# Kernel tuning notes

Hardware: AMD Instinct MI355X
Metric: run time of the kernel (lower is better)

The kernel has to match this reference:

```python
import jax, jax.numpy as jnp
import numpy as np

B, NMAX, H, C, HID = 256, 512, 256, 64, 512
NEG = jnp.float32(-1e9)

def setup_inputs() -> dict:
    key = jax.random.key(0)
    ks = jax.random.split(key, 12)
    s_in = 1.0 / np.sqrt(2 * H + C)
    s_h = 1.0 / np.sqrt(HID)
    return {
        "nodes_hv": jax.random.normal(ks[0], (B, NMAX, H), jnp.float32),
        "class_cond": jax.random.normal(ks[1], (B, C), jnp.float32),
        "W1": jax.random.normal(ks[2], (2 * H + C, HID), jnp.float32) * s_in,
        "b1": jnp.zeros((HID,), jnp.float32),
        "W2": jax.random.normal(ks[3], (HID, HID), jnp.float32) * s_h,
        "b2": jnp.zeros((HID,), jnp.float32),
        "W3": jax.random.normal(ks[4], (HID, 1), jnp.float32) * s_h,
        "b3": jnp.zeros((1,), jnp.float32),
        "dirns": jax.random.randint(ks[5], (B,), 0, 2, jnp.int32),
        "node_counts": jax.random.randint(ks[6], (B,), NMAX // 2 + 1, NMAX, jnp.int32),
        "dests": jax.random.randint(ks[7], (B,), 0, NMAX // 2, jnp.int32),
    }

def reference(nodes_hv, class_cond, W1, b1, W2, b2, W3, b3, dirns, node_counts, dests):
    Bb, Nmax, Hh = nodes_hv.shape
    D = Nmax - 1  # padded number of candidate destinations
    # per-graph newest node embedding: hv[b, n_b - 1]
    src_idx = (node_counts - 1).astype(jnp.int32)
    src_embed = jnp.take_along_axis(nodes_hv, src_idx[:, None, None], axis=1)  # [B,1,H]
    src_b = jnp.broadcast_to(src_embed, (Bb, D, Hh))
    cand = nodes_hv[:, :D, :]  # candidate (old-node) embeddings, padded
    # dirn == 1: edge new->old, so (src_side, dest_side) = (cand, new); else (new, cand)
    dirn1 = (dirns == 1)[:, None, None]
    side_a = jnp.where(dirn1, cand, src_b)
    side_b = jnp.where(dirn1, src_b, cand)
    cc = jnp.broadcast_to(class_cond[:, None, :], (Bb, D, class_cond.shape[-1]))
    x = jnp.concatenate([side_a, side_b, cc], axis=2)  # [B, D, 2H+C]
    h = jax.nn.relu(jnp.einsum("bdi,ih->bdh", x, W1) + b1)
    h = jax.nn.relu(jnp.einsum("bdi,ih->bdh", h, W2) + b2)
    scores = (jnp.einsum("bdi,io->bdo", h, W3) + b3)[..., 0]  # [B, D]
    # ragged validity: graph b has n_b - 1 candidates
    valid = jnp.arange(D)[None, :] < (node_counts - 1)[:, None]
    scores = jnp.where(valid, scores, NEG)
    logp = jax.nn.log_softmax(scores, axis=1)
    loss = -jnp.take_along_axis(logp, dests[:, None].astype(jnp.int32), axis=1)[:, 0]  # [B]
    return loss
```

## Files before the change

### kernel.cpp

```cpp
#include <hip/hip_runtime.h>
#include <math.h>

#define BB    256
#define NMAX  512
#define HH    256
#define CC    64
#define HID   512
#define NEGV  -1000000000.0f
#define MT    64
#define NW    8
#define SA_LD 258
#define TILE  512
#define KSTR  (16 * TILE)

typedef __attribute__((ext_vector_type(8)))  short  short8;
typedef __attribute__((ext_vector_type(16))) float  floatx16;

__device__ inline ushort f2bf(float x) {
    unsigned u = __float_as_uint(x);
    u = (u + 0x7FFFu + ((u >> 16) & 1u)) >> 16;
    return (ushort)u;
}

__global__ __launch_bounds__(256) void prep_kernel(
    const float* __restrict__ W1, const float* __restrict__ W2,
    ushort* __restrict__ Wt1s, ushort* __restrict__ Wt2s,
    const float* __restrict__ nodes_hv, const float* __restrict__ class_cond,
    const float* __restrict__ b1,
    const int* __restrict__ dirns, const int* __restrict__ node_counts,
    float* __restrict__ v_ws)
{
    const int blk = blockIdx.x;
    const int t = threadIdx.x;

    __shared__ float s_conv[32][68];
    __shared__ float s_src[HH];
    __shared__ float s_cc[CC];

    if (blk < 256) {
        const float* W = (blk < 128) ? W1 : W2;
        ushort* out    = (blk < 128) ? Wt1s : Wt2s;
        const int bb  = blk & 127;
        const int kb  = bb >> 3, ntg = bb & 7;

        {
            const int kl = t >> 3, nn = (t & 7) * 8;
            const float* src = W + (size_t)(kb * 32 + kl) * HID + ntg * 64 + nn;
            *(float4*)&s_conv[kl][nn]     = *(const float4*)src;
            *(float4*)&s_conv[kl][nn + 4] = *(const float4*)(src + 4);
        }
        __syncthreads();

        const int tile_l = t >> 6, ls = t & 63;
        const int kh_l = tile_l >> 1, nt_l = tile_l & 1;
        const int q5s = ls >> 5, l31s = ls & 31;
        short8 o;
        #pragma unroll
        for (int j = 0; j < 8; ++j)
            o[j] = (short)f2bf(s_conv[kh_l * 16 + q5s * 8 + j][nt_l * 32 + l31s]);
        const int kh = kb * 2 + kh_l, nt = ntg * 2 + nt_l;
        *(short8*)(out + ((size_t)kh * 16 + nt) * TILE + ls * 8) = o;
    } else {
        const int b = blk - 256;
        const int nc   = node_counts[b];
        const int dirn = dirns[b];
        const int src_idx = nc - 1;

        s_src[t] = nodes_hv[((size_t)b * NMAX + src_idx) * HH + t];
        if (t < CC) s_cc[t] = class_cond[b * CC + t];
        __syncthreads();

        const int srcoff = (dirn == 1) ? HH : 0;

        const int j = 2 * t;
        float acc0 = b1[j];
        float acc1 = b1[j + 1];

        #pragma unroll 4
        for (int r = 0; r < HH; ++r) {
            const float s = s_src[r];
            const float* wp = W1 + (size_t)(srcoff + r) * HID + j;
            acc0 += s * wp[0];
            acc1 += s * wp[1];
        }
        #pragma unroll 4
        for (int c = 0; c < CC; ++c) {
            const float s = s_cc[c];
            const float* wp = W1 + (size_t)(2 * HH + c) * HID + j;
            acc0 += s * wp[0];
            acc1 += s * wp[1];
        }
        v_ws[b * HID + j]     = acc0;
        v_ws[b * HID + j + 1] = acc1;
    }
}

__global__ __launch_bounds__(512, 4) void mlp2(
    const float* __restrict__ nodes_hv,
    const ushort* __restrict__ Wt1s, const ushort* __restrict__ Wt2s,
    const float* __restrict__ b2, const float* __restrict__ W3,
    const float* __restrict__ b3,
    const int* __restrict__ dirns, const int* __restrict__ node_counts,
    const float* __restrict__ v_ws, float* __restrict__ scores)
{
    const int b  = blockIdx.y;
    const int d0 = blockIdx.x * MT;
    const int t  = threadIdx.x;
    const int lane = t & 63, wv = t >> 6;
    const int l31 = lane & 31, q5 = lane >> 5;

    __shared__ ushort s_u[32768];

    const int nc = node_counts[b];

    if (d0 >= nc - 1) {
        if (t < MT) scores[b * NMAX + d0 + t] = NEGV;
        return;
    }

    const int kh0 = (dirns[b] == 1) ? 0 : 16;

    {
        const float4* src4 = (const float4*)nodes_hv + ((size_t)b * NMAX + d0) * (HH / 4);
        #pragma unroll
        for (int i = 0; i < (MT * HH / 4) / 512; ++i) {
            int idx = t + i * 512;
            int row = idx >> 6, c4 = idx & 63;
            float4 v = src4[idx];
            ushort4 p;
            p.x = f2bf(v.x); p.y = f2bf(v.y); p.z = f2bf(v.z); p.w = f2bf(v.w);
            *(ushort4*)&s_u[row * SA_LD + c4 * 4] = p;
        }
    }
    __syncthreads();

    floatx16 acc[2][2];
    #pragma unroll
    for (int mt = 0; mt < 2; ++mt)
        #pragma unroll
        for (int nt = 0; nt < 2; ++nt)
            #pragma unroll
            for (int r = 0; r < 16; ++r)
                acc[mt][nt][r] = 0.f;

    {
        const ushort* wb1 = Wt1s + ((size_t)kh0 * 16 + wv * 2) * TILE + lane * 8;
        #pragma unroll
        for (int kh = 0; kh < 16; ++kh) {
            const ushort* wp = wb1 + (size_t)kh * KSTR;
            short8 b0 = *(const short8*)(wp);
            short8 b1f = *(const short8*)(wp + TILE);
            short8 a0 = *(const short8*)&s_u[(l31)      * SA_LD + kh * 16 + q5 * 8];
            short8 a1 = *(const short8*)&s_u[(32 + l31) * SA_LD + kh * 16 + q5 * 8];
            acc[0][0] = __builtin_amdgcn_mfma_f32_32x32x16_bf16(a0, b0,  acc[0][0], 0, 0, 0);
            acc[0][1] = __builtin_amdgcn_mfma_f32_32x32x16_bf16(a0, b1f, acc[0][1], 0, 0, 0);
            acc[1][0] = __builtin_amdgcn_mfma_f32_32x32x16_bf16(a1, b0,  acc[1][0], 0, 0, 0);
            acc[1][1] = __builtin_amdgcn_mfma_f32_32x32x16_bf16(a1, b1f, acc[1][1], 0, 0, 0);
        }
    }
    __syncthreads();

    {
        #pragma unroll
        for (int nt = 0; nt < 2; ++nt) {
            const int n = wv * 64 + nt * 32 + l31;
            const float v = v_ws[b * HID + n];
            const int kh2 = n >> 4;
            const int q2p = (n >> 3) & 1;
            const int j_w = n & 7;
            #pragma unroll
            for (int mt = 0; mt < 2; ++mt) {
                #pragma unroll
                for (int reg = 0; reg < 16; ++reg) {
                    const int l31w = (reg & 3) + 8 * (reg >> 2) + 4 * q5;
                    float h = acc[mt][nt][reg] + v;
                    h = h > 0.f ? h : 0.f;
                    s_u[((kh2 * 2 + mt) * 64 + q2p * 32 + l31w) * 8 + j_w] = f2bf(h);
                }
            }
        }
    }
    __syncthreads();

    #pragma unroll
    for (int mt = 0; mt < 2; ++mt)
        #pragma unroll
        for (int nt = 0; nt < 2; ++nt)
            #pragma unroll
            for (int r = 0; r < 16; ++r)
                acc[mt][nt][r] = 0.f;
    {
        const ushort* wb2 = Wt2s + ((size_t)wv * 2) * TILE + lane * 8;
        #pragma unroll
        for (int kh2 = 0; kh2 < 32; ++kh2) {
            const ushort* wp = wb2 + (size_t)kh2 * KSTR;
            short8 b0 = *(const short8*)(wp);
            short8 b1f = *(const short8*)(wp + TILE);
            short8 a0 = *(const short8*)&s_u[((kh2 * 2 + 0) * 64 + lane) * 8];
            short8 a1 = *(const short8*)&s_u[((kh2 * 2 + 1) * 64 + lane) * 8];
            acc[0][0] = __builtin_amdgcn_mfma_f32_32x32x16_bf16(a0, b0,  acc[0][0], 0, 0, 0);
            acc[0][1] = __builtin_amdgcn_mfma_f32_32x32x16_bf16(a0, b1f, acc[0][1], 0, 0, 0);
            acc[1][0] = __builtin_amdgcn_mfma_f32_32x32x16_bf16(a1, b0,  acc[1][0], 0, 0, 0);
            acc[1][1] = __builtin_amdgcn_mfma_f32_32x32x16_bf16(a1, b1f, acc[1][1], 0, 0, 0);
        }
    }

    float p[2][16];
    #pragma unroll
    for (int mt = 0; mt < 2; ++mt)
        #pragma unroll
        for (int r = 0; r < 16; ++r)
            p[mt][r] = 0.f;
    #pragma unroll
    for (int nt = 0; nt < 2; ++nt) {
        const int n  = wv * 64 + nt * 32 + l31;
        const float bb = b2[n];
        const float w3 = W3[n];
        #pragma unroll
        for (int mt = 0; mt < 2; ++mt)
            #pragma unroll
            for (int r = 0; r < 16; ++r) {
                float h = acc[mt][nt][r] + bb;
                h = h > 0.f ? h : 0.f;
                p[mt][r] += h * w3;
            }
    }
    __syncthreads();
    float* s_red = (float*)s_u;
    #pragma unroll
    for (int mt = 0; mt < 2; ++mt)
        #pragma unroll
        for (int r = 0; r < 16; ++r) {
            float v = p[mt][r];
            v += __shfl_xor(v, 1, 64);
            v += __shfl_xor(v, 2, 64);
            v += __shfl_xor(v, 4, 64);
            v += __shfl_xor(v, 8, 64);
            v += __shfl_xor(v, 16, 64);
            if (l31 == 0) {
                const int row = mt * 32 + (r & 3) + 8 * (r >> 2) + 4 * q5;
                s_red[wv * MT + row] = v;
            }
        }
    __syncthreads();
    if (t < MT) {
        float s = b3[0];
        #pragma unroll
        for (int w = 0; w < NW; ++w) s += s_red[w * MT + t];
        const int d = d0 + t;
        scores[b * NMAX + d] = (d < nc - 1) ? s : NEGV;
    }
}

__global__ __launch_bounds__(256) void loss_kernel(
    const float* __restrict__ scores, const int* __restrict__ dests,
    float* __restrict__ out)
{
    const int b = blockIdx.x;
    const int t = threadIdx.x;
    __shared__ float red[4];

    const float s0 = scores[b * NMAX + t];
    const float s1 = scores[b * NMAX + t + 256];

    const int lane = t & 63, wv = t >> 6;

    float mx = fmaxf(s0, s1);
    #pragma unroll
    for (int off = 32; off > 0; off >>= 1) mx = fmaxf(mx, __shfl_down(mx, off, 64));
    if (lane == 0) red[wv] = mx;
    __syncthreads();
    mx = fmaxf(fmaxf(red[0], red[1]), fmaxf(red[2], red[3]));
    __syncthreads();

    float e = __expf(s0 - mx) + __expf(s1 - mx);
    #pragma unroll
    for (int off = 32; off > 0; off >>= 1) e += __shfl_down(e, off, 64);
    if (lane == 0) red[wv] = e;
    __syncthreads();

    if (t == 0) {
        const float sum = red[0] + red[1] + red[2] + red[3];
        const float sd = scores[b * NMAX + dests[b]];
        out[b] = -(sd - mx - logf(sum));
    }
}

extern "C" void kernel_launch(void* const* d_in, const int* in_sizes, int n_in,
                              void* d_out, int out_size, void* d_ws, size_t ws_size,
                              hipStream_t stream) {
    const float* nodes_hv    = (const float*)d_in[0];
    const float* class_cond  = (const float*)d_in[1];
    const float* W1          = (const float*)d_in[2];
    const float* b1          = (const float*)d_in[3];
    const float* W2          = (const float*)d_in[4];
    const float* b2          = (const float*)d_in[5];
    const float* W3          = (const float*)d_in[6];
    const float* b3          = (const float*)d_in[7];
    const int*   dirns       = (const int*)d_in[8];
    const int*   node_counts = (const int*)d_in[9];
    const int*   dests       = (const int*)d_in[10];
    float* out = (float*)d_out;

    ushort* Wt1s   = (ushort*)d_ws;
    ushort* Wt2s   = Wt1s + 32 * KSTR;
    float*  v_ws   = (float*)(Wt2s + 32 * KSTR);
    float*  scores = v_ws + BB * HID;

    prep_kernel<<<512, 256, 0, stream>>>(W1, W2, Wt1s, Wt2s,
                                         nodes_hv, class_cond, b1,
                                         dirns, node_counts, v_ws);
    mlp2<<<dim3(NMAX / MT, BB), 512, 0, stream>>>(
        nodes_hv, Wt1s, Wt2s, b2, W3, b3, dirns, node_counts, v_ws, scores);
    loss_kernel<<<BB, 256, 0, stream>>>(scores, dests, out);
}
```

Baseline: 337.0 us.

## Rewarp MFMA tiling to 1x4 per wave, swizzle LDS, split prep GEMV

After: 342.7 us. About the same (+1.7%).

```diff
diff --git a/kernel.cpp b/kernel.cpp
--- a/kernel.cpp
+++ b/kernel.cpp
@@ -9,7 +9,7 @@
 #define NEGV  -1000000000.0f
 #define MT    64
 #define NW    8
-#define SA_LD 258
+#define SA_LD 264
 #define TILE  512
 #define KSTR  (16 * TILE)
 
@@ -26,16 +26,14 @@
     const float* __restrict__ W1, const float* __restrict__ W2,
     ushort* __restrict__ Wt1s, ushort* __restrict__ Wt2s,
     const float* __restrict__ nodes_hv, const float* __restrict__ class_cond,
-    const float* __restrict__ b1,
     const int* __restrict__ dirns, const int* __restrict__ node_counts,
-    float* __restrict__ v_ws)
+    float* __restrict__ v_part)
 {
     const int blk = blockIdx.x;
     const int t = threadIdx.x;
 
     __shared__ float s_conv[32][68];
-    __shared__ float s_src[HH];
-    __shared__ float s_cc[CC];
+    __shared__ float vals[160];
 
     if (blk < 256) {
         const float* W = (blk < 128) ? W1 : W2;
@@ -61,53 +59,53 @@
         const int kh = kb * 2 + kh_l, nt = ntg * 2 + nt_l;
         *(short8*)(out + ((size_t)kh * 16 + nt) * TILE + ls * 8) = o;
     } else {
-        const int b = blk - 256;
+        const int idx = blk - 256;
+        const int b = idx >> 1, seg = idx & 1;
+        const int r0 = seg * 160;
+
         const int nc   = node_counts[b];
         const int dirn = dirns[b];
         const int src_idx = nc - 1;
-
-        s_src[t] = nodes_hv[((size_t)b * NMAX + src_idx) * HH + t];
-        if (t < CC) s_cc[t] = class_cond[b * CC + t];
+        const int srcoff = (dirn == 1) ? HH : 0;
+
+        if (t < 160) {
+            const int r = r0 + t;
+            vals[t] = (r < HH)
+                ? nodes_hv[((size_t)b * NMAX + src_idx) * HH + r]
+                : class_cond[b * CC + (r - HH)];
+        }
         __syncthreads();
 
-        const int srcoff = (dirn == 1) ? HH : 0;
-
         const int j = 2 * t;
-        float acc0 = b1[j];
-        float acc1 = b1[j + 1];
-
+        float acc0 = 0.f, acc1 = 0.f;
         #pragma unroll 4
-        for (int r = 0; r < HH; ++r) {
-            const float s = s_src[r];
-            const float* wp = W1 + (size_t)(srcoff + r) * HID + j;
-            acc0 += s * wp[0];
-            acc1 += s * wp[1];
-        }
-        #pragma unroll 4
-        for (int c = 0; c < CC; ++c) {
-            const float s = s_cc[c];
-            const float* wp = W1 + (size_t)(2 * HH + c) * HID + j;
-            acc0 += s * wp[0];
-            acc1 += s * wp[1];
-        }
-        v_ws[b * HID + j]     = acc0;
-        v_ws[b * HID + j + 1] = acc1;
+        for (int i = 0; i < 160; ++i) {
+            const int r = r0 + i;
+            const int wrow = (r < HH) ? (srcoff + r) : (2 * HH + (r - HH));
+            const float* wp = W1 + (size_t)wrow * HID + j;
+            acc0 += vals[i] * wp[0];
+            acc1 += vals[i] * wp[1];
+        }
+        v_part[((size_t)seg * BB + b) * HID + j]     = acc0;
+        v_part[((size_t)seg * BB + b) * HID + j + 1] = acc1;
     }
 }
 
 __global__ __launch_bounds__(512, 4) void mlp2(
     const float* __restrict__ nodes_hv,
     const ushort* __restrict__ Wt1s, const ushort* __restrict__ Wt2s,
-    const float* __restrict__ b2, const float* __restrict__ W3,
-    const float* __restrict__ b3,
+    const float* __restrict__ b1, const float* __restrict__ b2,
+    const float* __restrict__ W3, const float* __restrict__ b3,
     const int* __restrict__ dirns, const int* __restrict__ node_counts,
-    const float* __restrict__ v_ws, float* __restrict__ scores)
+    const float* __restrict__ v_part, float* __restrict__ scores)
 {
     const int b  = blockIdx.y;
     const int d0 = blockIdx.x * MT;
     const int t  = threadIdx.x;
     const int lane = t & 63, wv = t >> 6;
     const int l31 = lane & 31, q5 = lane >> 5;
+    const int mt  = wv & 1;
+    const int nc4 = wv >> 1;
 
     __shared__ ushort s_u[32768];
 
@@ -134,119 +132,112 @@
     }
     __syncthreads();
 
-    floatx16 acc[2][2];
-    #pragma unroll
-    for (int mt = 0; mt < 2; ++mt)
-        #pragma unroll
-        for (int nt = 0; nt < 2; ++nt)
-            #pragma unroll
-            for (int r = 0; r < 16; ++r)
-                acc[mt][nt][r] = 0.f;
+    floatx16 acc[4];
+    #pragma unroll
+    for (int nt = 0; nt < 4; ++nt)
+        #pragma unroll
+        for (int r = 0; r < 16; ++r)
+            acc[nt][r] = 0.f;
 
     {
-        const ushort* wb1 = Wt1s + ((size_t)kh0 * 16 + wv * 2) * TILE + lane * 8;
+        const ushort* wb1 = Wt1s + ((size_t)kh0 * 16 + nc4 * 4) * TILE + lane * 8;
         #pragma unroll
         for (int kh = 0; kh < 16; ++kh) {
             const ushort* wp = wb1 + (size_t)kh * KSTR;
-            short8 b0 = *(const short8*)(wp);
-            short8 b1f = *(const short8*)(wp + TILE);
-            short8 a0 = *(const short8*)&s_u[(l31)      * SA_LD + kh * 16 + q5 * 8];
-            short8 a1 = *(const short8*)&s_u[(32 + l31) * SA_LD + kh * 16 + q5 * 8];
-            acc[0][0] = __builtin_amdgcn_mfma_f32_32x32x16_bf16(a0, b0,  acc[0][0], 0, 0, 0);
-            acc[0][1] = __builtin_amdgcn_mfma_f32_32x32x16_bf16(a0, b1f, acc[0][1], 0, 0, 0);
-            acc[1][0] = __builtin_amdgcn_mfma_f32_32x32x16_bf16(a1, b0,  acc[1][0], 0, 0, 0);
-            acc[1][1] = __builtin_amdgcn_mfma_f32_32x32x16_bf16(a1, b1f, acc[1][1], 0, 0, 0);
+            short8 bf0 = *(const short8*)(wp);
+            short8 bf1 = *(const short8*)(wp + TILE);
+            short8 bf2 = *(const short8*)(wp + 2 * TILE);
+            short8 bf3 = *(const short8*)(wp + 3 * TILE);
+            short8 a = *(const short8*)&s_u[(mt * 32 + l31) * SA_LD + kh * 16 + q5 * 8];
+            acc[0] = __builtin_amdgcn_mfma_f32_32x32x16_bf16(a, bf0, acc[0], 0, 0, 0);
+            acc[1] = __builtin_amdgcn_mfma_f32_32x32x16_bf16(a, bf1, acc[1], 0, 0, 0);
+            acc[2] = __builtin_amdgcn_mfma_f32_32x32x16_bf16(a, bf2, acc[2], 0, 0, 0);
+            acc[3] = __builtin_amdgcn_mfma_f32_32x32x16_bf16(a, bf3, acc[3], 0, 0, 0);
         }
     }
     __syncthreads();
 
     {
         #pragma unroll
-        for (int nt = 0; nt < 2; ++nt) {
-            const int n = wv * 64 + nt * 32 + l31;
-            const float v = v_ws[b * HID + n];
+        for (int nt = 0; nt < 4; ++nt) {
+            const int n = nc4 * 128 + nt * 32 + l31;
+            const float v = b1[n] + v_part[(size_t)b * HID + n]
+                          + v_part[((size_t)BB + b) * HID + n];
             const int kh2 = n >> 4;
             const int q2p = (n >> 3) & 1;
             const int j_w = n & 7;
+            const int fxor = ((kh2 & 1) << 1) ^ q2p;
             #pragma unroll
-            for (int mt = 0; mt < 2; ++mt) {
-                #pragma unroll
-                for (int reg = 0; reg < 16; ++reg) {
-                    const int l31w = (reg & 3) + 8 * (reg >> 2) + 4 * q5;
-                    float h = acc[mt][nt][reg] + v;
-                    h = h > 0.f ? h : 0.f;
-                    s_u[((kh2 * 2 + mt) * 64 + q2p * 32 + l31w) * 8 + j_w] = f2bf(h);
-                }
+            for (int reg = 0; reg < 16; ++reg) {
+                const int row31w = (reg & 3) + 8 * (reg >> 2) + 4 * q5;
+                float h = acc[nt][reg] + v;
+                h = h > 0.f ? h : 0.f;
+                const int slot = (kh2 * 2 + mt) * 64 + q2p * 32 + (row31w ^ fxor);
+                s_u[slot * 8 + j_w] = f2bf(h);
             }
         }
     }
     __syncthreads();
 
     #pragma unroll
-    for (int mt = 0; mt < 2; ++mt)
-        #pragma unroll
-        for (int nt = 0; nt < 2; ++nt)
-            #pragma unroll
-            for (int r = 0; r < 16; ++r)
-                acc[mt][nt][r] = 0.f;
+    for (int nt = 0; nt < 4; ++nt)
+        #pragma unroll
+        for (int r = 0; r < 16; ++r)
+            acc[nt][r] = 0.f;
     {
-        const ushort* wb2 = Wt2s + ((size_t)wv * 2) * TILE + lane * 8;
+        const ushort* wb2 = Wt2s + ((size_t)nc4 * 4) * TILE + lane * 8;
         #pragma unroll
         for (int kh2 = 0; kh2 < 32; ++kh2) {
             const ushort* wp = wb2 + (size_t)kh2 * KSTR;
-            short8 b0 = *(const short8*)(wp);
-            short8 b1f = *(const short8*)(wp + TILE);
-            short8 a0 = *(const short8*)&s_u[((kh2 * 2 + 0) * 64 + lane) * 8];
-            short8 a1 = *(const short8*)&s_u[((kh2 * 2 + 1) * 64 + lane) * 8];
-            acc[0][0] = __builtin_amdgcn_mfma_f32_32x32x16_bf16(a0, b0,  acc[0][0], 0, 0, 0);
-            acc[0][1] = __builtin_amdgcn_mfma_f32_32x32x16_bf16(a0, b1f, acc[0][1], 0, 0, 0);
-            acc[1][0] = __builtin_amdgcn_mfma_f32_32x32x16_bf16(a1, b0,  acc[1][0], 0, 0, 0);
-            acc[1][1] = __builtin_amdgcn_mfma_f32_32x32x16_bf16(a1, b1f, acc[1][1], 0, 0, 0);
-        }
-    }
-
-    float p[2][16];
-    #pragma unroll
-    for (int mt = 0; mt < 2; ++mt)
-        #pragma unroll
-        for (int r = 0; r < 16; ++r)
-            p[mt][r] = 0.f;
-    #pragma unroll
-    for (int nt = 0; nt < 2; ++nt) {
-        const int n  = wv * 64 + nt * 32 + l31;
+            short8 bf0 = *(const short8*)(wp);
+            short8 bf1 = *(const short8*)(wp + TILE);
+            short8 bf2 = *(const short8*)(wp + 2 * TILE);
+            short8 bf3 = *(const short8*)(wp + 3 * TILE);
+            const int slot = (kh2 * 2 + mt) * 64 + q5 * 32
+                           + (l31 ^ ((kh2 & 1) << 1) ^ q5);
+            short8 a = *(const short8*)&s_u[slot * 8];
+            acc[0] = __builtin_amdgcn_mfma_f32_32x32x16_bf16(a, bf0, acc[0], 0, 0, 0);
+            acc[1] = __builtin_amdgcn_mfma_f32_32x32x16_bf16(a, bf1, acc[1], 0, 0, 0);
+            acc[2] = __builtin_amdgcn_mfma_f32_32x32x16_bf16(a, bf2, acc[2], 0, 0, 0);
+            acc[3] = __builtin_amdgcn_mfma_f32_32x32x16_bf16(a, bf3, acc[3], 0, 0, 0);
+        }
+    }
+
+    float p[16];
+    #pragma unroll
+    for (int r = 0; r < 16; ++r) p[r] = 0.f;
+    #pragma unroll
+    for (int nt = 0; nt < 4; ++nt) {
+        const int n  = nc4 * 128 + nt * 32 + l31;
         const float bb = b2[n];
         const float w3 = W3[n];
         #pragma unroll
-        for (int mt = 0; mt < 2; ++mt)
-            #pragma unroll
-            for (int r = 0; r < 16; ++r) {
-                float h = acc[mt][nt][r] + bb;
-                h = h > 0.f ? h : 0.f;
-                p[mt][r] += h * w3;
-            }
+        for (int r = 0; r < 16; ++r) {
+            float h = acc[nt][r] + bb;
+            h = h > 0.f ? h : 0.f;
+            p[r] += h * w3;
+        }
     }
     __syncthreads();
     float* s_red = (float*)s_u;
     #pragma unroll
-    for (int mt = 0; mt < 2; ++mt)
-        #pragma unroll
-        for (int r = 0; r < 16; ++r) {
-            float v = p[mt][r];
-            v += __shfl_xor(v, 1, 64);
-            v += __shfl_xor(v, 2, 64);
-            v += __shfl_xor(v, 4, 64);
-            v += __shfl_xor(v, 8, 64);
-            v += __shfl_xor(v, 16, 64);
-            if (l31 == 0) {
-                const int row = mt * 32 + (r & 3) + 8 * (r >> 2) + 4 * q5;
-                s_red[wv * MT + row] = v;
-            }
-        }
+    for (int r = 0; r < 16; ++r) {
+        float v = p[r];
+        v += __shfl_xor(v, 1, 64);
+        v += __shfl_xor(v, 2, 64);
+        v += __shfl_xor(v, 4, 64);
+        v += __shfl_xor(v, 8, 64);
+        v += __shfl_xor(v, 16, 64);
+        if (l31 == 0) {
+            const int row = mt * 32 + (r & 3) + 8 * (r >> 2) + 4 * q5;
+            s_red[nc4 * MT + row] = v;
+        }
+    }
     __syncthreads();
     if (t < MT) {
         float s = b3[0];
         #pragma unroll
-        for (int w = 0; w < NW; ++w) s += s_red[w * MT + t];
+        for (int c = 0; c < 4; ++c) s += s_red[c * MT + t];
         const int d = d0 + t;
         scores[b * NMAX + d] = (d < nc - 1) ? s : NEGV;
     }
@@ -304,13 +295,13 @@
 
     ushort* Wt1s   = (ushort*)d_ws;
     ushort* Wt2s   = Wt1s + 32 * KSTR;
-    float*  v_ws   = (float*)(Wt2s + 32 * KSTR);
-    float*  scores = v_ws + BB * HID;
-
-    prep_kernel<<<512, 256, 0, stream>>>(W1, W2, Wt1s, Wt2s,
-                                         nodes_hv, class_cond, b1,
-                                         dirns, node_counts, v_ws);
+    float*  v_part = (float*)(Wt2s + 32 * KSTR);
+    float*  scores = v_part + 2 * BB * HID;
+
+    prep_kernel<<<768, 256, 0, stream>>>(W1, W2, Wt1s, Wt2s,
+                                         nodes_hv, class_cond,
+                                         dirns, node_counts, v_part);
     mlp2<<<dim3(NMAX / MT, BB), 512, 0, stream>>>(
-        nodes_hv, Wt1s, Wt2s, b2, W3, b3, dirns, node_counts, v_ws, scores);
+        nodes_hv, Wt1s, Wt2s, b1, b2, W3, b3, dirns, node_counts, v_part, scores);
     loss_kernel<<<BB, 256, 0, stream>>>(scores, dests, out);
 }
```
